# Kernel tuning notes

Hardware: AMD Instinct MI355X
Metric: run time of the kernel (lower is better)

Reference implementation:

```python
import jax, jax.numpy as jnp
import numpy as np

EMBED_DIM = 1024
N_HEADS = 16
HEAD_DIM = EMBED_DIM // N_HEADS


def setup_inputs() -> dict:
    key = jax.random.key(0)
    ks = jax.random.split(key, 8)
    B, Tq, Tk, C = 2, 2048, 2048, EMBED_DIM
    s = 1.0 / np.sqrt(C)
    return {
        "query": jax.random.normal(ks[0], (B, Tq, C), jnp.float32),
        "context": jax.random.normal(ks[1], (B, Tk, C), jnp.float32),
        "Wq": jax.random.normal(ks[2], (C, C), jnp.float32) * s,
        "bq": jnp.zeros((C,), jnp.float32),
        "Wkv": jax.random.normal(ks[3], (C, 2 * C), jnp.float32) * s,
        "bkv": jnp.zeros((2 * C,), jnp.float32),
        "Wo": jax.random.normal(ks[4], (C, C), jnp.float32) * s,
        "bo": jnp.zeros((C,), jnp.float32),
    }


def reference(query, context, Wq, bq, Wkv, bkv, Wo, bo):
    B, Tq, C = query.shape
    Tk = context.shape[1]
    H, D = N_HEADS, HEAD_DIM
    # projections
    q = (query @ Wq + bq).reshape(B, Tq, H, D)        # [B,Tq,H,D]
    kv = (context @ Wkv + bkv).reshape(B, Tk, 2, H, D)
    k = kv[:, :, 0]                                   # [B,Tk,H,D]
    v = kv[:, :, 1]
    scale = D ** -0.5
    # attention scores [B,H,Tq,Tk]
    attn = jnp.einsum("bqhd,bkhd->bhqk", q, k) * scale
    attn = jax.nn.softmax(attn, axis=-1)
    # dropout p=0.0 -> identity in eval / p=0
    out = jnp.einsum("bhqk,bkhd->bqhd", attn, v).reshape(B, Tq, C)
    return out @ Wo + bo
```

## Files before the change

### kernel.cpp

```cpp
#include <hip/hip_runtime.h>
#include <math.h>

typedef unsigned short u16;
typedef unsigned int u32;
typedef __attribute__((ext_vector_type(8))) short short8;
typedef __attribute__((ext_vector_type(4))) short short4v;
typedef __attribute__((ext_vector_type(4))) float f32x4;

__device__ __forceinline__ u16 f2bf(float f) {
  union { float f; unsigned u; } x; x.f = f;
  unsigned r = x.u + 0x7FFFu + ((x.u >> 16) & 1u);
  return (u16)(r >> 16);
}

__device__ __forceinline__ u32 asu(float f) {
  union { float f; u32 u; } x; x.f = f; return x.u;
}

__device__ __forceinline__ u32 pack2bf(float a, float b) {
  return __builtin_amdgcn_perm(asu(b) + 0x8000u, asu(a) + 0x8000u, 0x07060302u);
}

__device__ __forceinline__ void gld_lds16(const void* g, void* l) {
  __builtin_amdgcn_global_load_lds(
      (const __attribute__((address_space(1))) unsigned int*)g,
      (__attribute__((address_space(3))) unsigned int*)l, 16, 0, 0);
}

__global__ void pre_kernel(const float* __restrict__ q, const float* __restrict__ c,
                           const float* __restrict__ Wq, const float* __restrict__ Wkv,
                           const float* __restrict__ Wo,
                           u16* __restrict__ xq, u16* __restrict__ xc,
                           u16* __restrict__ WqF, u16* __restrict__ WkvF,
                           u16* __restrict__ WoF) {
  __shared__ float tile[32][33];
  int bx = blockIdx.x;
  int t = threadIdx.y * 32 + threadIdx.x;
  if (bx < 8192) {
    int i = bx * 256 + t;
    const float* src = q; u16* dst = xq;
    if (i >= 1048576) { i -= 1048576; src = c; dst = xc; }
    float4 v = ((const float4*)src)[i];
    ((uint2*)dst)[i] = make_uint2(
        (unsigned)f2bf(v.x) | ((unsigned)f2bf(v.y) << 16),
        (unsigned)f2bf(v.z) | ((unsigned)f2bf(v.w) << 16));
  } else {
    int g = bx - 8192;
    int gx = g & 127, gy = g >> 7;
    const float* src; u16* dst; int N, n0;
    if (gx < 32)      { src = Wq;  dst = WqF;  N = 1024; n0 = gx * 32; }
    else if (gx < 96) { src = Wkv; dst = WkvF; N = 2048; n0 = (gx - 32) * 32; }
    else              { src = Wo;  dst = WoF;  N = 1024; n0 = (gx - 96) * 32; }
    int k0 = gy * 32;
    int tx = threadIdx.x, ty = threadIdx.y;
#pragma unroll
    for (int i = 0; i < 4; ++i)
      tile[ty * 4 + i][tx] = src[(size_t)(k0 + ty * 4 + i) * N + n0 + tx];
    __syncthreads();
    int e = t * 4;
    int ch = e >> 9, rem = e & 511;
    int kg = (rem >> 7) & 3;
    int nl = (rem >> 3) & 15;
    int j0 = rem & 7;
    int kk = kg * 8 + j0;
    int nn = ch * 16 + nl;
    u32 lo = pack2bf(tile[kk][nn], tile[kk + 1][nn]);
    u32 hi = pack2bf(tile[kk + 2][nn], tile[kk + 3][nn]);
    *(uint2*)(dst + (size_t)(((n0 >> 4) + ch) * 32 + gy) * 512 + rem) = make_uint2(lo, hi);
  }
}

__global__ __launch_bounds__(256) void qkv_gemm(
    const u16* __restrict__ Xq, const u16* __restrict__ Xc,
    const u16* __restrict__ WqF, const u16* __restrict__ WkvF,
    const float* __restrict__ bq, const float* __restrict__ bkv,
    u16* __restrict__ qb, u16* __restrict__ kf, u16* __restrict__ vf,
    float qscale) {
  __shared__ __align__(16) u16 smem[16896];
  const int tid = threadIdx.x, lane = tid & 63, wave = tid >> 6;
  const int quad = lane >> 4, cl = lane & 15;
  const int wr = (wave >> 1) * 64, wc = (wave & 1) * 64;

  int x = blockIdx.x;
  const u16 *A, *Bf; const float* bias; int m0, n0; bool isq;
  if (x < 256) {
    isq = true;  A = Xq; Bf = WqF;  bias = bq;
    m0 = (x >> 3) * 128; n0 = (x & 7) * 128;
  } else {
    isq = false; x -= 256; A = Xc; Bf = WkvF; bias = bkv;
    m0 = (x >> 4) * 128; n0 = (x & 15) * 128;
  }
  const int bn4 = (n0 + wc) >> 4;

  const int rA = lane >> 3;
  const int kcs = ((lane & 7) ^ rA) * 8;
  const int r7 = cl & 7;

  auto stageA = [&](int k0, int buf) {
    u16* As = smem + buf * 8192;
#pragma unroll
    for (int it = 0; it < 4; ++it) {
      int chunk = it * 4 + wave;
      gld_lds16(A + (size_t)(m0 + chunk * 8 + rA) * 1024 + k0 + kcs, As + chunk * 512);
    }
  };

  f32x4 acc[4][4] = {};

  stageA(0, 0);
  __syncthreads();

  for (int i = 0; i < 16; ++i) {
    const int k0 = i * 64;
    const int cur = i & 1;
    if (i < 15) stageA(k0 + 64, cur ^ 1);
    const u16* As = smem + cur * 8192;
    short8 bf[2][4];
#pragma unroll
    for (int ks = 0; ks < 2; ++ks)
#pragma unroll
      for (int ni = 0; ni < 4; ++ni)
        bf[ks][ni] = *(const short8*)(Bf + (size_t)((bn4 + ni) * 32 + (k0 >> 5) + ks) * 512 + lane * 8);
#pragma unroll
    for (int ks = 0; ks < 2; ++ks) {
      short8 af[4];
#pragma unroll
      for (int mi = 0; mi < 4; ++mi) {
        int row = wr + mi * 16 + cl;
        af[mi] = *(const short8*)(As + (row >> 3) * 512 + r7 * 64 +
                                  (((ks << 2) | quad) ^ r7) * 8);
      }
#pragma unroll
      for (int mi = 0; mi < 4; ++mi)
#pragma unroll
        for (int ni = 0; ni < 4; ++ni)
          acc[mi][ni] = __builtin_amdgcn_mfma_f32_16x16x32_bf16(af[mi], bf[ks][ni], acc[mi][ni], 0, 0, 0);
    }
    __syncthreads();
  }

  if (isq) {
#pragma unroll
    for (int mi = 0; mi < 4; ++mi)
#pragma unroll
      for (int ni = 0; ni < 4; ++ni)
#pragma unroll
        for (int r = 0; r < 4; ++r) {
          int row = m0 + wr + mi * 16 + quad * 4 + r;
          int col = n0 + wc + ni * 16 + cl;
          qb[(size_t)row * 1024 + col] = f2bf((acc[mi][ni][r] + bias[col]) * qscale);
        }
    return;
  }

  const int b = m0 >> 11, kt0 = (m0 & 2047) >> 6;
  const bool kreg = (n0 < 1024);
  if (kreg) {
#pragma unroll
    for (int mi = 0; mi < 4; ++mi)
#pragma unroll
      for (int ni = 0; ni < 4; ++ni)
#pragma unroll
        for (int r = 0; r < 4; ++r)
          smem[(wr + mi * 16 + quad * 4 + r) * 132 + wc + ni * 16 + cl] =
              f2bf(acc[mi][ni][r] + bias[n0 + wc + ni * 16 + cl]);
    __syncthreads();
#pragma unroll
    for (int i = 0; i < 8; ++i) {
      int c = i * 4 + wave;
      int hs = c >> 4, ts = (c >> 3) & 1, ks = (c >> 2) & 1, idx = c & 3;
      int h = (n0 >> 6) + hs;
      size_t bhkt = ((size_t)((b * 16 + h) * 32 + kt0 + ts)) * 4096;
      short8 v = *(const short8*)(smem + (ts * 64 + idx * 16 + cl) * 132 +
                                  hs * 64 + ks * 32 + quad * 8);
      *(short8*)(kf + bhkt + (size_t)(ks * 4 + idx) * 512 + lane * 8) = v;
    }
  } else {
#pragma unroll
    for (int mi = 0; mi < 4; ++mi)
#pragma unroll
      for (int ni = 0; ni < 4; ++ni) {
        float v0 = acc[mi][ni][0] + bias[n0 + wc + ni * 16 + cl];
        float v1 = acc[mi][ni][1] + bias[n0 + wc + ni * 16 + cl];
        float v2 = acc[mi][ni][2] + bias[n0 + wc + ni * 16 + cl];
        float v3 = acc[mi][ni][3] + bias[n0 + wc + ni * 16 + cl];
        *(uint2*)(smem + (wc + ni * 16 + cl) * 132 + wr + mi * 16 + quad * 4) =
            make_uint2(pack2bf(v0, v1), pack2bf(v2, v3));
      }
    __syncthreads();
#pragma unroll
    for (int i = 0; i < 8; ++i) {
      int c = i * 4 + wave;
      int hs = c >> 4, ts = (c >> 3) & 1, ks = (c >> 2) & 1, idx = c & 3;
      int h = ((n0 - 1024) >> 6) + hs;
      size_t bhkt = ((size_t)((b * 16 + h) * 32 + kt0 + ts)) * 4096;
      const u16* src = smem + (hs * 64 + idx * 16 + cl) * 132 + ts * 64 + ks * 32 + quad * 4;
      short8 v;
      *(short4v*)&v       = *(const short4v*)(src);
      *((short4v*)&v + 1) = *(const short4v*)(src + 16);
      *(short8*)(vf + bhkt + (size_t)(ks * 4 + idx) * 512 + lane * 8) = v;
    }
  }
}

__global__ __launch_bounds__(256) void o_gemm(
    const u16* __restrict__ A, const u16* __restrict__ Bf,
    const float* __restrict__ bias, float* __restrict__ Cm) {
  __shared__ __align__(16) u16 As[2][64 * 64];
  const int tid = threadIdx.x, lane = tid & 63, wave = tid >> 6;
  const int quad = lane >> 4, cl = lane & 15;
  const int m0 = (blockIdx.x >> 3) * 64, n0 = (blockIdx.x & 7) * 128;
  const int wr = (wave >> 1) * 32, wc = (wave & 1) * 64;
  const int bn4 = (n0 + wc) >> 4;

  const int rA = lane >> 3;
  const int kcs = ((lane & 7) ^ rA) * 8;
  const int r7 = cl & 7;

  auto stageA = [&](int k0, int buf) {
#pragma unroll
    for (int it = 0; it < 2; ++it) {
      int chunk = wave * 2 + it;
      gld_lds16(A + (size_t)(m0 + chunk * 8 + rA) * 1024 + k0 + kcs, As[buf] + chunk * 512);
    }
  };

  f32x4 acc[2][4] = {};

  stageA(0, 0);
  __syncthreads();

  for (int i = 0; i < 16; ++i) {
    const int k0 = i * 64;
    const int cur = i & 1;
    if (i < 15) stageA(k0 + 64, cur ^ 1);
    short8 bf[2][4];
#pragma unroll
    for (int ks = 0; ks < 2; ++ks)
#pragma unroll
      for (int ni = 0; ni < 4; ++ni)
        bf[ks][ni] = *(const short8*)(Bf + (size_t)((bn4 + ni) * 32 + (k0 >> 5) + ks) * 512 + lane * 8);
#pragma unroll
    for (int ks = 0; ks < 2; ++ks) {
      short8 af[2];
#pragma unroll
      for (int mi = 0; mi < 2; ++mi) {
        int row = wr + mi * 16 + cl;
        af[mi] = *(const short8*)(As[cur] + (row >> 3) * 512 + r7 * 64 +
                                  (((ks << 2) | quad) ^ r7) * 8);
      }
#pragma unroll
      for (int mi = 0; mi < 2; ++mi)
#pragma unroll
        for (int ni = 0; ni < 4; ++ni)
          acc[mi][ni] = __builtin_amdgcn_mfma_f32_16x16x32_bf16(af[mi], bf[ks][ni], acc[mi][ni], 0, 0, 0);
    }
    __syncthreads();
  }
#pragma unroll
  for (int mi = 0; mi < 2; ++mi)
#pragma unroll
    for (int ni = 0; ni < 4; ++ni)
#pragma unroll
      for (int r = 0; r < 4; ++r) {
        int row = m0 + wr + mi * 16 + quad * 4 + r;
        int col = n0 + wc + ni * 16 + cl;
        Cm[(size_t)row * 1024 + col] = acc[mi][ni][r] + bias[col];
      }
}

__global__ __launch_bounds__(256, 4) void flash_attn(
    const u16* __restrict__ qb, const u16* __restrict__ kf,
    const u16* __restrict__ vf, u16* __restrict__ outp) {
  __shared__ __align__(16) u16 kv[2][16 * 512];
  const int tid = threadIdx.x, lane = tid & 63, wave = tid >> 6;
  const int quad = lane >> 4, cl = lane & 15;
  const int id = blockIdx.x;
  const int h = (id & 7) | (((id >> 3) & 1) << 3);
  const int b = (id >> 4) & 1;
  const int qt = id >> 5;

  const int qrow0 = b * 2048 + qt * 64 + wave * 16;
  short8 bq[2];
#pragma unroll
  for (int ks = 0; ks < 2; ++ks)
    bq[ks] = *(const short8*)(qb + (size_t)(qrow0 + cl) * 1024 + h * 64 + ks * 32 + quad * 8);

  const u16* kfb = kf + (size_t)((b * 16 + h) * 32) * 4096;
  const u16* vfb = vf + (size_t)((b * 16 + h) * 32) * 4096;

  auto stage = [&](int kt, int buf) {
#pragma unroll
    for (int i = 0; i < 2; ++i) {
      int c = wave * 2 + i;
      gld_lds16(kfb + (size_t)kt * 4096 + c * 512 + lane * 8, &kv[buf][c * 512]);
      gld_lds16(vfb + (size_t)kt * 4096 + c * 512 + lane * 8, &kv[buf][(8 + c) * 512]);
    }
  };

  f32x4 o_acc[4] = {};
  float l_lane = 0.f;

  stage(0, 0);
  __syncthreads();

#pragma unroll 1
  for (int kt = 0; kt < 32; ++kt) {
    const int cur = kt & 1, nxt = cur ^ 1;
    if (kt < 31) stage(kt + 1, nxt);
    const u16* kb = &kv[cur][0];
    const u16* vb = &kv[cur][8 * 512];
    f32x4 st[4] = {};
#pragma unroll
    for (int ks = 0; ks < 2; ++ks)
#pragma unroll
      for (int ni = 0; ni < 4; ++ni) {
        short8 ak = *(const short8*)(kb + (ks * 4 + ni) * 512 + lane * 8);
        st[ni] = __builtin_amdgcn_mfma_f32_16x16x32_bf16(ak, bq[ks], st[ni], 0, 0, 0);
      }
    u32 bp[2][4];
#pragma unroll
    for (int ni = 0; ni < 4; ++ni) {
      float p0 = __builtin_amdgcn_exp2f(st[ni][0]);
      float p1 = __builtin_amdgcn_exp2f(st[ni][1]);
      float p2 = __builtin_amdgcn_exp2f(st[ni][2]);
      float p3 = __builtin_amdgcn_exp2f(st[ni][3]);
      l_lane += (p0 + p1) + (p2 + p3);
      bp[ni >> 1][(ni & 1) * 2 + 0] = pack2bf(p0, p1);
      bp[ni >> 1][(ni & 1) * 2 + 1] = pack2bf(p2, p3);
    }
#pragma unroll
    for (int ks = 0; ks < 2; ++ks) {
      short8 pb;
      *(u32*)&pb     = bp[ks][0];
      ((u32*)&pb)[1] = bp[ks][1];
      ((u32*)&pb)[2] = bp[ks][2];
      ((u32*)&pb)[3] = bp[ks][3];
#pragma unroll
      for (int nd = 0; nd < 4; ++nd) {
        short8 av = *(const short8*)(vb + (ks * 4 + nd) * 512 + lane * 8);
        o_acc[nd] = __builtin_amdgcn_mfma_f32_16x16x32_bf16(av, pb, o_acc[nd], 0, 0, 0);
      }
    }
    __syncthreads();
  }
  l_lane += __shfl_xor(l_lane, 16);
  l_lane += __shfl_xor(l_lane, 32);
  float inv = 1.f / l_lane;
  u16* Ow = &kv[0][wave * 16 * 68];
#pragma unroll
  for (int nd = 0; nd < 4; ++nd)
#pragma unroll
    for (int r2 = 0; r2 < 2; ++r2)
      *(u32*)(Ow + cl * 68 + nd * 16 + quad * 4 + r2 * 2) =
          pack2bf(o_acc[nd][r2 * 2] * inv, o_acc[nd][r2 * 2 + 1] * inv);
#pragma unroll
  for (int half = 0; half < 2; ++half) {
    int row = half * 8 + (lane >> 3);
    int d0 = (lane & 7) * 8;
    short8 ov = *(const short8*)(Ow + row * 68 + d0);
    *(short8*)(outp + (size_t)(qrow0 + row) * 1024 + h * 64 + d0) = ov;
  }
}

extern "C" void kernel_launch(void* const* d_in, const int* in_sizes, int n_in,
                              void* d_out, int out_size, void* d_ws, size_t ws_size,
                              hipStream_t stream) {
  const float* query   = (const float*)d_in[0];
  const float* context = (const float*)d_in[1];
  const float* Wq  = (const float*)d_in[2];
  const float* bq  = (const float*)d_in[3];
  const float* Wkv = (const float*)d_in[4];
  const float* bkv = (const float*)d_in[5];
  const float* Wo  = (const float*)d_in[6];
  const float* bo  = (const float*)d_in[7];
  float* out = (float*)d_out;

  char* ws = (char*)d_ws;
  size_t off = 0;
  auto alloc = [&](size_t bytes) {
    char* p = ws + off;
    off += (bytes + 255) & ~(size_t)255;
    return p;
  };
  u16* buf0 = (u16*)alloc(4096ull * 1024 * 2);
  u16* xcb  = (u16*)alloc(4096ull * 1024 * 2);
  u16* WqF  = (u16*)alloc(1024ull * 1024 * 2);
  u16* WkvF = (u16*)alloc(2048ull * 1024 * 2);
  u16* WoF  = (u16*)alloc(1024ull * 1024 * 2);
  u16* qb   = (u16*)alloc(4096ull * 1024 * 2);
  u16* kfr  = (u16*)alloc(4ull * 1024 * 1024 * 2);
  u16* vfr  = (u16*)alloc(4ull * 1024 * 1024 * 2);

  const float QSCALE = 0.125f * 1.44269504f;

  pre_kernel<<<12288, dim3(32, 8), 0, stream>>>(query, context, Wq, Wkv, Wo,
                                                buf0, xcb, WqF, WkvF, WoF);
  qkv_gemm<<<768, 256, 0, stream>>>(buf0, xcb, WqF, WkvF, bq, bkv,
                                    qb, kfr, vfr, QSCALE);
  flash_attn<<<1024, 256, 0, stream>>>(qb, kfr, vfr, buf0);
  o_gemm<<<512, 256, 0, stream>>>(buf0, WoF, bo, out);
}
```

Measured before the change: 206.4 us.

## Compute softmax row sums with MFMA and tighten the flash-attention inner loop

The per-lane scalar accumulation of the softmax denominator, and its cross-lane shuffles, are replaced by an extra MFMA that multiplies a ones vector by the packed bf16 probabilities. The denominator now comes directly from the matrix unit for each query column. The change also hoists the V tile LDS reads ahead of the exp computation, swaps the manual bf16 packing for the hardware v_cvt_pk_bf16_f32 instruction, and raises wave priority around the MFMA blocks with s_setprio. The aim is to cut VALU work and expose more overlap between LDS reads, exp and MFMA. In exchange the denominator is summed from bf16-rounded probabilities, the extra MFMA adds matrix-unit work, and holding the V fragments in registers raises register pressure.

```diff
diff --git a/kernel.cpp b/kernel.cpp
--- a/kernel.cpp
+++ b/kernel.cpp
@@ -19,6 +19,12 @@
 
 __device__ __forceinline__ u32 pack2bf(float a, float b) {
   return __builtin_amdgcn_perm(asu(b) + 0x8000u, asu(a) + 0x8000u, 0x07060302u);
+}
+
+__device__ __forceinline__ u32 cvtpk2bf(float a, float b) {
+  u32 r;
+  asm("v_cvt_pk_bf16_f32 %0, %1, %2" : "=v"(r) : "v"(a), "v"(b));
+  return r;
 }
 
 __device__ __forceinline__ void gld_lds16(const void* g, void* l) {
@@ -286,6 +292,10 @@
   for (int ks = 0; ks < 2; ++ks)
     bq[ks] = *(const short8*)(qb + (size_t)(qrow0 + cl) * 1024 + h * 64 + ks * 32 + quad * 8);
 
+  short8 ones;
+#pragma unroll
+  for (int j = 0; j < 8; ++j) ones[j] = (short)0x3F80;
+
   const u16* kfb = kf + (size_t)((b * 16 + h) * 32) * 4096;
   const u16* vfb = vf + (size_t)((b * 16 + h) * 32) * 4096;
 
@@ -299,7 +309,7 @@
   };
 
   f32x4 o_acc[4] = {};
-  float l_lane = 0.f;
+  f32x4 l_acc = {};
 
   stage(0, 0);
   __syncthreads();
@@ -311,6 +321,7 @@
     const u16* kb = &kv[cur][0];
     const u16* vb = &kv[cur][8 * 512];
     f32x4 st[4] = {};
+    __builtin_amdgcn_s_setprio(1);
 #pragma unroll
     for (int ks = 0; ks < 2; ++ks)
 #pragma unroll
@@ -318,6 +329,13 @@
         short8 ak = *(const short8*)(kb + (ks * 4 + ni) * 512 + lane * 8);
         st[ni] = __builtin_amdgcn_mfma_f32_16x16x32_bf16(ak, bq[ks], st[ni], 0, 0, 0);
       }
+    __builtin_amdgcn_s_setprio(0);
+    short8 av[2][4];
+#pragma unroll
+    for (int ks = 0; ks < 2; ++ks)
+#pragma unroll
+      for (int nd = 0; nd < 4; ++nd)
+        av[ks][nd] = *(const short8*)(vb + (ks * 4 + nd) * 512 + lane * 8);
     u32 bp[2][4];
 #pragma unroll
     for (int ni = 0; ni < 4; ++ni) {
@@ -325,10 +343,10 @@
       float p1 = __builtin_amdgcn_exp2f(st[ni][1]);
       float p2 = __builtin_amdgcn_exp2f(st[ni][2]);
       float p3 = __builtin_amdgcn_exp2f(st[ni][3]);
-      l_lane += (p0 + p1) + (p2 + p3);
-      bp[ni >> 1][(ni & 1) * 2 + 0] = pack2bf(p0, p1);
-      bp[ni >> 1][(ni & 1) * 2 + 1] = pack2bf(p2, p3);
-    }
+      bp[ni >> 1][(ni & 1) * 2 + 0] = cvtpk2bf(p0, p1);
+      bp[ni >> 1][(ni & 1) * 2 + 1] = cvtpk2bf(p2, p3);
+    }
+    __builtin_amdgcn_s_setprio(1);
 #pragma unroll
     for (int ks = 0; ks < 2; ++ks) {
       short8 pb;
@@ -337,23 +355,21 @@
       ((u32*)&pb)[2] = bp[ks][2];
       ((u32*)&pb)[3] = bp[ks][3];
 #pragma unroll
-      for (int nd = 0; nd < 4; ++nd) {
-        short8 av = *(const short8*)(vb + (ks * 4 + nd) * 512 + lane * 8);
-        o_acc[nd] = __builtin_amdgcn_mfma_f32_16x16x32_bf16(av, pb, o_acc[nd], 0, 0, 0);
-      }
-    }
-    __syncthreads();
-  }
-  l_lane += __shfl_xor(l_lane, 16);
-  l_lane += __shfl_xor(l_lane, 32);
-  float inv = 1.f / l_lane;
+      for (int nd = 0; nd < 4; ++nd)
+        o_acc[nd] = __builtin_amdgcn_mfma_f32_16x16x32_bf16(av[ks][nd], pb, o_acc[nd], 0, 0, 0);
+      l_acc = __builtin_amdgcn_mfma_f32_16x16x32_bf16(ones, pb, l_acc, 0, 0, 0);
+    }
+    __builtin_amdgcn_s_setprio(0);
+    __syncthreads();
+  }
+  float inv = 1.f / l_acc[0];
   u16* Ow = &kv[0][wave * 16 * 68];
 #pragma unroll
   for (int nd = 0; nd < 4; ++nd)
 #pragma unroll
     for (int r2 = 0; r2 < 2; ++r2)
       *(u32*)(Ow + cl * 68 + nd * 16 + quad * 4 + r2 * 2) =
-          pack2bf(o_acc[nd][r2 * 2] * inv, o_acc[nd][r2 * 2 + 1] * inv);
+          cvtpk2bf(o_acc[nd][r2 * 2] * inv, o_acc[nd][r2 * 2 + 1] * inv);
 #pragma unroll
   for (int half = 0; half < 2; ++half) {
     int row = half * 8 + (lane >> 3);
```

After: 198.9 us. -3.6%, faster.
